# Optimization experiments

Hardware: AMD Instinct MI355X
Metric: run time of the kernel (lower is better)

Reference implementation:

```python
import jax, jax.numpy as jnp
import numpy as np

DIM = 128
N_CENTERS = 30
CUT_LO, CUT_HI = 0.0, 10.0
N_CONV = 3
NODE_VOCAB = 100
EDGE_VOCAB = 500
N_NODES = 50000
N_EDGES = 800000
N_GRAPHS = 100
DIM_E = DIM + N_CENTERS  # 158


def setup_inputs() -> dict:
    key = jax.random.key(0)
    ks = jax.random.split(key, 20)
    def xav(k, shape):
        fan_in = shape[-2] if len(shape) >= 2 else shape[-1]
        return (jax.random.normal(k, shape, dtype=jnp.float32) / np.sqrt(fan_in)).astype(jnp.float32)
    inp = {
        'node_types': jax.random.randint(ks[0], (N_NODES,), 0, NODE_VOCAB),
        'edge_types': jax.random.randint(ks[1], (N_EDGES,), 0, EDGE_VOCAB),
        'src': jax.random.randint(ks[2], (N_EDGES,), 0, N_NODES),
        'dst': jax.random.randint(ks[3], (N_EDGES,), 0, N_NODES),
        'graph_ids': jnp.sort(jax.random.randint(ks[4], (N_NODES,), 0, N_GRAPHS)),
        'distances': jax.random.uniform(ks[5], (N_EDGES,), dtype=jnp.float32, minval=CUT_LO, maxval=CUT_HI),
        'n_graphs': N_GRAPHS,
        # embedding tables
        'node_emb': xav(ks[6], (NODE_VOCAB, DIM)),
        'edge_emb': xav(ks[7], (EDGE_VOCAB, DIM)),
        # stacked per-conv-layer weights (n_conv leading dim)
        'Wn1': xav(ks[8], (N_CONV, DIM, DIM)),  'bn1': jnp.zeros((N_CONV, DIM), jnp.float32),
        'Wn2': xav(ks[9], (N_CONV, DIM, DIM)),  'bn2': jnp.zeros((N_CONV, DIM), jnp.float32),
        'We1': xav(ks[10], (N_CONV, DIM_E, DIM)), 'be1': jnp.zeros((N_CONV, DIM), jnp.float32),
        'We2': xav(ks[11], (N_CONV, DIM, DIM)),  'be2': jnp.zeros((N_CONV, DIM), jnp.float32),
        'Wc':  xav(ks[12], (N_CONV, DIM, DIM)),  'bc': jnp.zeros((N_CONV, DIM), jnp.float32),
        # read layer
        'Wr1': xav(ks[13], (DIM, DIM)), 'br1': jnp.zeros((DIM,), jnp.float32),
        'Wr2': xav(ks[14], (DIM, 1)),   'br2': jnp.zeros((1,), jnp.float32),
    }
    return inp


def reference(node_types, edge_types, src, dst, graph_ids, distances, n_graphs,
              node_emb, edge_emb, Wn1, bn1, Wn2, bn2, We1, be1, We2, be2, Wc, bc,
              Wr1, br1, Wr2, br2):
    # embeddings
    h = node_emb[node_types]                      # [N, D]
    e_emb = edge_emb[edge_types]                  # [E, D]
    # RBF expansion of distances
    centers = jnp.linspace(CUT_LO, CUT_HI, N_CENTERS, dtype=jnp.float32)
    gap = centers[1] - centers[0]
    rbf = jnp.exp(-((distances[:, None] - centers[None, :]) ** 2) / gap)  # [E, n_centers]
    e = jnp.concatenate([e_emb, rbf], axis=1)     # [E, D + n_centers]

    n_nodes = h.shape[0]
    for i in range(N_CONV):
        node_path = jnp.maximum(h[src] @ Wn1[i] + bn1[i], 0.0) @ Wn2[i] + bn2[i]   # [E, D]
        edge_path = jnp.maximum(e @ We1[i] + be1[i], 0.0) @ We2[i] + be2[i]        # [E, D]
        m = jnp.tanh((node_path * edge_path) @ Wc[i] + bc[i])                       # [E, D]
        h = h + jax.ops.segment_sum(m, dst, num_segments=n_nodes)                   # scatter-add to dst

    # readout MLP + per-graph node sum
    hr = jnp.maximum(h @ Wr1 + br1, 0.0) @ Wr2 + br2                                # [N, 1]
    out = jax.ops.segment_sum(hr, graph_ids, num_segments=n_graphs)                 # [G, 1]
    return out.reshape(-1)
```

## Files before the change

### kernel.cpp

```cpp
#include <hip/hip_runtime.h>
#include <stdint.h>

#define NNODES 50000
#define NEDGES 800000
#define NGRAPH 100
#define NCHUNK (NEDGES / 16)
#define NWAVES 4096

typedef _Float16 f16;
typedef __attribute__((ext_vector_type(8))) _Float16 half8;
typedef __attribute__((ext_vector_type(4))) _Float16 half4;
typedef __attribute__((ext_vector_type(4))) float floatx4;

__device__ __forceinline__ void stage_WT(const float* __restrict__ W, f16* WT,
                                         int tid, int nthr) {
    for (int idx = tid; idx < 128 * 32; idx += nthr) {
        int k = idx >> 5, n4 = (idx & 31) * 4;
        floatx4 v = *(const floatx4*)(W + k * 128 + n4);
        WT[(n4 + 0) * 136 + k] = (f16)v[0];
        WT[(n4 + 1) * 136 + k] = (f16)v[1];
        WT[(n4 + 2) * 136 + k] = (f16)v[2];
        WT[(n4 + 3) * 136 + k] = (f16)v[3];
    }
}

__device__ __forceinline__ float fast_tanh(float x) {
    x = fminf(fmaxf(x, -15.0f), 15.0f);
    float e2 = __expf(2.0f * x);
    return (e2 - 1.0f) * __builtin_amdgcn_rcpf(e2 + 1.0f);
}

__device__ __forceinline__ int mtAddr(int c, int rgroup) {
    return c * 16 + ((((c >> 2) + rgroup) & 3) << 2);
}

__global__ void init_k(float* out, int osz, int* cnt) {
    int i = blockIdx.x * 256 + threadIdx.x;
    if (i < osz) out[i] = 0.0f;
    if (i < NNODES) cnt[i] = 0;
}

__global__ void hist_k(const int* __restrict__ dst, int* __restrict__ cnt) {
    int e = blockIdx.x * 256 + threadIdx.x;
    if (e < NEDGES) atomicAdd(&cnt[dst[e]], 1);
}

__global__ __launch_bounds__(1024) void scan1_k(const int* __restrict__ cnt,
                                                int* __restrict__ rowStart,
                                                int* __restrict__ blockSum) {
    __shared__ int buf[1024];
    int tid = threadIdx.x;
    int i = blockIdx.x * 1024 + tid;
    int v = (i < NNODES) ? cnt[i] : 0;
    buf[tid] = v;
    __syncthreads();
    for (int off = 1; off < 1024; off <<= 1) {
        int t = (tid >= off) ? buf[tid - off] : 0;
        __syncthreads();
        buf[tid] += t;
        __syncthreads();
    }
    if (i < NNODES) rowStart[i] = buf[tid] - v;
    if (tid == 1023) blockSum[blockIdx.x] = buf[1023];
}

__global__ void scan2_k(int* __restrict__ blockSum, int nb) {
    if (threadIdx.x == 0) {
        int run = 0;
        for (int b = 0; b < nb; ++b) { int s = blockSum[b]; blockSum[b] = run; run += s; }
    }
}

__global__ __launch_bounds__(1024) void scan3_k(int* __restrict__ rowStart,
                                                const int* __restrict__ blockSum,
                                                int* __restrict__ cnt) {
    int i = blockIdx.x * 1024 + threadIdx.x;
    if (i < NNODES) { rowStart[i] += blockSum[blockIdx.x]; cnt[i] = 0; }
    if (i == 0) rowStart[NNODES] = NEDGES;
}

__global__ void scatter_k(const int* __restrict__ src, const int* __restrict__ et,
                          const int* __restrict__ dst, const float* __restrict__ dist,
                          const int* __restrict__ rowStart, int* __restrict__ cnt,
                          uint4* __restrict__ packE) {
    int e = blockIdx.x * 256 + threadIdx.x;
    if (e >= NEDGES) return;
    int d = dst[e];
    int pos = rowStart[d] + atomicAdd(&cnt[d], 1);
    uint4 pk;
    pk.x = (unsigned)src[e];
    pk.y = (unsigned)et[e];
    pk.z = (unsigned)d;
    pk.w = __float_as_uint(dist[e]);
    packE[pos] = pk;
}

__global__ void gather_h(const int* __restrict__ nt, const float* __restrict__ emb,
                         float* __restrict__ h) {
    int i = blockIdx.x * 256 + threadIdx.x;
    int row = i >> 5, c4 = (i & 31) * 4;
    if (row < NNODES)
        *(floatx4*)(h + row * 128 + c4) = *(const floatx4*)(emb + nt[row] * 128 + c4);
}

template <int MODE>
__global__ __launch_bounds__(1024, 4) void mlp_kernel(
        const float* __restrict__ X, int M,
        const float* __restrict__ W1, const float* __restrict__ b1,
        const float* __restrict__ W2, const float* __restrict__ b2,
        f16* __restrict__ Out) {
    __shared__ f16 W1T[128 * 136];
    __shared__ f16 W2T[(MODE == 0) ? 128 * 136 : 8];
    __shared__ f16 xBuf[256 * 136];
    __shared__ float bias1[128];
    __shared__ float bias2[128];
    int tid = threadIdx.x;

    stage_WT(W1, W1T, tid, 1024);
    if (MODE == 0) stage_WT(W2, W2T, tid, 1024);
    if (tid < 128) { bias1[tid] = b1[tid]; bias2[tid] = (MODE == 0) ? b2[tid] : 0.0f; }

    int r0 = blockIdx.x * 256;
    for (int it = 0; it < 8; ++it) {
        int row = it * 32 + (tid >> 5);
        int c4 = (tid & 31) * 4;
        int gr = r0 + row;
        floatx4 x = {0.0f, 0.0f, 0.0f, 0.0f};
        if (gr < M) x = *(const floatx4*)(X + (size_t)gr * 128 + c4);
        f16* dph = xBuf + row * 136 + c4;
        dph[0] = (f16)x[0]; dph[1] = (f16)x[1]; dph[2] = (f16)x[2]; dph[3] = (f16)x[3];
    }
    __syncthreads();

    int lane = tid & 63, wv = tid >> 6;
    int R = wv * 16;
    int n16 = lane & 15, q = lane >> 4;

    half8 a[4];
    #pragma unroll
    for (int kk = 0; kk < 4; ++kk)
        a[kk] = *(const half8*)(xBuf + (R + n16) * 136 + kk * 32 + q * 8);

    floatx4 acc[8];
    #pragma unroll
    for (int f = 0; f < 8; ++f) {
        float bb = bias1[f * 16 + n16];
        acc[f] = (floatx4){bb, bb, bb, bb};
        #pragma unroll
        for (int kk = 0; kk < 4; ++kk) {
            half8 b = *(const half8*)(W1T + (f * 16 + n16) * 136 + kk * 32 + q * 8);
            acc[f] = __builtin_amdgcn_mfma_f32_16x16x32_f16(a[kk], b, acc[f], 0, 0, 0);
        }
    }

    if (MODE == 0) {
        #pragma unroll
        for (int f = 0; f < 8; ++f)
            #pragma unroll
            for (int i = 0; i < 4; ++i)
                xBuf[(R + q * 4 + i) * 136 + f * 16 + n16] = (f16)fmaxf(acc[f][i], 0.0f);
        #pragma unroll
        for (int kk = 0; kk < 4; ++kk)
            a[kk] = *(const half8*)(xBuf + (R + n16) * 136 + kk * 32 + q * 8);
        #pragma unroll
        for (int f = 0; f < 8; ++f) {
            float bb = bias2[f * 16 + n16];
            acc[f] = (floatx4){bb, bb, bb, bb};
            #pragma unroll
            for (int kk = 0; kk < 4; ++kk) {
                half8 b = *(const half8*)(W2T + (f * 16 + n16) * 136 + kk * 32 + q * 8);
                acc[f] = __builtin_amdgcn_mfma_f32_16x16x32_f16(a[kk], b, acc[f], 0, 0, 0);
            }
        }
        #pragma unroll
        for (int f = 0; f < 8; ++f)
            #pragma unroll
            for (int i = 0; i < 4; ++i) {
                int gr = r0 + R + q * 4 + i;
                if (gr < M) Out[(size_t)gr * 128 + f * 16 + n16] = (f16)acc[f][i];
            }
    } else {
        #pragma unroll
        for (int f = 0; f < 8; ++f)
            #pragma unroll
            for (int i = 0; i < 4; ++i) {
                int gr = r0 + R + q * 4 + i;
                if (gr < M) Out[(size_t)gr * 128 + f * 16 + n16] = (f16)acc[f][i];
            }
    }
}

__global__ __launch_bounds__(1024, 4) void edge_kernel(
        const uint4* __restrict__ packE,
        const f16* __restrict__ P, const f16* __restrict__ T,
        const float* __restrict__ We1,
        const float* __restrict__ We2, const float* __restrict__ be2,
        const float* __restrict__ Wc,  const float* __restrict__ bc,
        float* __restrict__ h) {
    __shared__ f16 W2T[128 * 136];
    __shared__ f16 WcT[128 * 136];
    __shared__ f16 W1rT[128 * 40];
    __shared__ f16 Uall[16 * 2176];
    __shared__ float sbe2[128], sbc[128];
    __shared__ int dstW[16][16];

    int tid = threadIdx.x;
    stage_WT(We2, W2T, tid, 1024);
    stage_WT(Wc,  WcT, tid, 1024);
    for (int idx = tid; idx < 128 * 32; idx += 1024) {
        int n = idx >> 5, kr = idx & 31;
        W1rT[n * 40 + kr] = (kr < 30) ? (f16)We1[(128 + kr) * 128 + n] : (f16)0.0f;
    }
    if (tid < 128) { sbe2[tid] = be2[tid]; sbc[tid] = bc[tid]; }
    __syncthreads();

    int lane = tid & 63, wv = tid >> 6;
    f16* U = Uall + wv * 2176;
    int* dW = dstW[wv];
    int n16 = lane & 15, q = lane >> 4;
    const float invgap = 29.0f / 10.0f;
    int colA = lane, colB = lane + 64;

    int wgid = blockIdx.x * 16 + wv;
    const int CPW = (NCHUNK + NWAVES - 1) / NWAVES;
    int c0 = wgid * CPW;
    int c1 = c0 + CPW; if (c1 > NCHUNK) c1 = NCHUNK;

    float carry0 = 0.0f, carry1 = 0.0f;
    int prev = -1;

    for (int ch = c0; ch < c1; ++ch) {
        int e0 = ch * 16;
        uint4 pk = {0u, 0u, 0u, 0u};
        if (lane < 16) pk = packE[e0 + lane];
        int   ety  = __shfl((int)pk.y, lane >> 2);
        int   srcv = __shfl((int)pk.x, n16);
        float d    = __shfl(__uint_as_float(pk.w), n16);
        if (lane < 16) dW[lane] = (int)pk.z;
        {
            int row = lane >> 2, sub = lane & 3;
            const uint4* Tp = (const uint4*)(T + (size_t)ety * 128 + sub * 32);
            uint4* ub = (uint4*)(U + row * 136 + sub * 32);
            ub[0] = Tp[0]; ub[1] = Tp[1]; ub[2] = Tp[2]; ub[3] = Tp[3];
        }
        half8 pA[4];
        {
            const f16* Pr = P + (size_t)srcv * 128 + q * 8;
            #pragma unroll
            for (int kk = 0; kk < 4; ++kk) pA[kk] = *(const half8*)(Pr + kk * 32);
        }

        {
            half8 ar;
            #pragma unroll
            for (int j = 0; j < 8; ++j) {
                int k = q * 8 + j;
                float c = (float)k * (10.0f / 29.0f);
                float df = d - c;
                ar[j] = (f16)((k < 30) ? __expf(-df * df * invgap) : 0.0f);
            }
            #pragma unroll
            for (int f = 0; f < 8; ++f) {
                int col = f * 16 + n16;
                floatx4 c4;
                #pragma unroll
                for (int i = 0; i < 4; ++i) c4[i] = (float)U[(q * 4 + i) * 136 + col];
                half8 br = *(const half8*)(W1rT + col * 40 + q * 8);
                c4 = __builtin_amdgcn_mfma_f32_16x16x32_f16(ar, br, c4, 0, 0, 0);
                #pragma unroll
                for (int i = 0; i < 4; ++i)
                    U[(q * 4 + i) * 136 + col] = (f16)fmaxf(c4[i], 0.0f);
            }
        }

        half8 a2[4];
        #pragma unroll
        for (int kk = 0; kk < 4; ++kk)
            a2[kk] = *(const half8*)(U + n16 * 136 + kk * 32 + q * 8);
        floatx4 ep[8];
        #pragma unroll
        for (int f = 0; f < 8; ++f) {
            float bb = sbe2[f * 16 + n16];
            ep[f] = (floatx4){bb, bb, bb, bb};
            #pragma unroll
            for (int kk = 0; kk < 4; ++kk) {
                half8 b = *(const half8*)(W2T + (f * 16 + n16) * 136 + kk * 32 + q * 8);
                ep[f] = __builtin_amdgcn_mfma_f32_16x16x32_f16(a2[kk], b, ep[f], 0, 0, 0);
            }
        }

        #pragma unroll
        for (int f = 0; f < 8; ++f) {
            int col = f * 16 + n16;
            #pragma unroll
            for (int i = 0; i < 4; ++i)
                U[(q * 4 + i) * 136 + col] = (f16)ep[f][i];
        }

        #pragma unroll
        for (int kk = 0; kk < 4; ++kk) {
            half8 pe = *(const half8*)(U + n16 * 136 + kk * 32 + q * 8);
            a2[kk] = pe * pA[kk];
        }
        floatx4 mm[8];
        #pragma unroll
        for (int f = 0; f < 8; ++f) {
            float bb = sbc[f * 16 + n16];
            mm[f] = (floatx4){bb, bb, bb, bb};
            #pragma unroll
            for (int kk = 0; kk < 4; ++kk) {
                half8 b = *(const half8*)(WcT + (f * 16 + n16) * 136 + kk * 32 + q * 8);
                mm[f] = __builtin_amdgcn_mfma_f32_16x16x32_f16(a2[kk], b, mm[f], 0, 0, 0);
            }
        }
        #pragma unroll
        for (int f = 0; f < 8; ++f) {
            int c = f * 16 + n16;
            half4 mv;
            #pragma unroll
            for (int i = 0; i < 4; ++i) mv[i] = (f16)fast_tanh(mm[f][i]);
            *(half4*)(U + mtAddr(c, q)) = mv;
        }

        {
            half4 va[4], vb[4];
            #pragma unroll
            for (int g2 = 0; g2 < 4; ++g2) {
                va[g2] = *(const half4*)(U + mtAddr(colA, g2));
                vb[g2] = *(const half4*)(U + mtAddr(colB, g2));
            }
            int dArr[16];
            *(int4*)(dArr)      = *(const int4*)(dW);
            *(int4*)(dArr + 4)  = *(const int4*)(dW + 4);
            *(int4*)(dArr + 8)  = *(const int4*)(dW + 8);
            *(int4*)(dArr + 12) = *(const int4*)(dW + 12);
            #pragma unroll
            for (int r = 0; r < 16; ++r) {
                int dd = dArr[r];
                float v0 = (float)va[r >> 2][r & 3];
                float v1 = (float)vb[r >> 2][r & 3];
                if (dd != prev) {
                    if (prev >= 0) {
                        unsafeAtomicAdd(&h[(size_t)prev * 128 + colA], carry0);
                        unsafeAtomicAdd(&h[(size_t)prev * 128 + colB], carry1);
                    }
                    prev = dd; carry0 = v0; carry1 = v1;
                } else { carry0 += v0; carry1 += v1; }
            }
        }
    }
    if (prev >= 0) {
        unsafeAtomicAdd(&h[(size_t)prev * 128 + colA], carry0);
        unsafeAtomicAdd(&h[(size_t)prev * 128 + colB], carry1);
    }
}

__global__ __launch_bounds__(1024, 4) void readout_k(
        const float* __restrict__ X, int M,
        const float* __restrict__ W1, const float* __restrict__ b1,
        const float* __restrict__ Wr2, const float* __restrict__ br2,
        const int* __restrict__ gid, float* __restrict__ out) {
    __shared__ f16 W1T[128 * 136];
    __shared__ f16 xBuf[256 * 136];
    __shared__ float bias1[128];
    __shared__ float sWr2[128];
    int tid = threadIdx.x;

    stage_WT(W1, W1T, tid, 1024);
    if (tid < 128) { bias1[tid] = b1[tid]; sWr2[tid] = Wr2[tid]; }

    int r0 = blockIdx.x * 256;
    for (int it = 0; it < 8; ++it) {
        int row = it * 32 + (tid >> 5);
        int c4 = (tid & 31) * 4;
        int gr = r0 + row;
        floatx4 x = {0.0f, 0.0f, 0.0f, 0.0f};
        if (gr < M) x = *(const floatx4*)(X + (size_t)gr * 128 + c4);
        f16* dph = xBuf + row * 136 + c4;
        dph[0] = (f16)x[0]; dph[1] = (f16)x[1]; dph[2] = (f16)x[2]; dph[3] = (f16)x[3];
    }
    __syncthreads();

    int lane = tid & 63, wv = tid >> 6;
    int R = wv * 16;
    int n16 = lane & 15, q = lane >> 4;

    half8 a[4];
    #pragma unroll
    for (int kk = 0; kk < 4; ++kk)
        a[kk] = *(const half8*)(xBuf + (R + n16) * 136 + kk * 32 + q * 8);

    floatx4 acc[8];
    #pragma unroll
    for (int f = 0; f < 8; ++f) {
        float bb = bias1[f * 16 + n16];
        acc[f] = (floatx4){bb, bb, bb, bb};
        #pragma unroll
        for (int kk = 0; kk < 4; ++kk) {
            half8 b = *(const half8*)(W1T + (f * 16 + n16) * 136 + kk * 32 + q * 8);
            acc[f] = __builtin_amdgcn_mfma_f32_16x16x32_f16(a[kk], b, acc[f], 0, 0, 0);
        }
    }

    float s[4];
    #pragma unroll
    for (int i = 0; i < 4; ++i) {
        float t = 0.0f;
        #pragma unroll
        for (int f = 0; f < 8; ++f)
            t += fmaxf(acc[f][i], 0.0f) * sWr2[f * 16 + n16];
        #pragma unroll
        for (int m = 1; m < 16; m <<= 1) t += __shfl_xor(t, m);
        s[i] = t;
    }

    if (n16 == 0) {
        float br2v = br2[0];
        float t = 0.0f; int g = -1;
        #pragma unroll
        for (int i = 0; i < 4; ++i) {
            int gr = r0 + R + q * 4 + i;
            if (gr < M) {
                int gi = gid[gr];
                float si = s[i] + br2v;
                if (gi == g) t += si;
                else { if (g >= 0) unsafeAtomicAdd(&out[g], t); g = gi; t = si; }
            }
        }
        if (g >= 0) unsafeAtomicAdd(&out[g], t);
    }
}

extern "C" void kernel_launch(void* const* d_in, const int* in_sizes, int n_in,
                              void* d_out, int out_size, void* d_ws, size_t ws_size,
                              hipStream_t stream) {
    (void)in_sizes; (void)n_in; (void)ws_size;
    const int*   node_types = (const int*)d_in[0];
    const int*   edge_types = (const int*)d_in[1];
    const int*   src        = (const int*)d_in[2];
    const int*   dst        = (const int*)d_in[3];
    const int*   graph_ids  = (const int*)d_in[4];
    const float* distances  = (const float*)d_in[5];
    const float* node_emb   = (const float*)d_in[7];
    const float* edge_emb   = (const float*)d_in[8];
    const float* Wn1 = (const float*)d_in[9];
    const float* bn1 = (const float*)d_in[10];
    const float* Wn2 = (const float*)d_in[11];
    const float* bn2 = (const float*)d_in[12];
    const float* We1 = (const float*)d_in[13];
    const float* be1 = (const float*)d_in[14];
    const float* We2 = (const float*)d_in[15];
    const float* be2 = (const float*)d_in[16];
    const float* Wc  = (const float*)d_in[17];
    const float* bc  = (const float*)d_in[18];
    const float* Wr1 = (const float*)d_in[19];
    const float* br1 = (const float*)d_in[20];
    const float* Wr2 = (const float*)d_in[21];
    const float* br2 = (const float*)d_in[22];

    char* w = (char*)d_ws;
    auto carve = [&](size_t bytes) { char* p = w; w += (bytes + 255) & ~(size_t)255; return p; };
    float* h        = (float*)carve((size_t)NNODES * 128 * 4);
    f16*   P        = (f16*)  carve((size_t)NNODES * 128 * 2);
    f16*   T        = (f16*)  carve((size_t)500 * 128 * 2);
    int*   rowStart = (int*)  carve((size_t)(NNODES + 1) * 4);
    int*   cnt      = (int*)  carve((size_t)NNODES * 4);
    int*   blockSum = (int*)  carve((size_t)64 * 4);
    uint4* packE    = (uint4*)carve((size_t)NEDGES * 16);

    float* out = (float*)d_out;
    const int NB1 = (NNODES + 1023) / 1024;

    init_k<<<(NNODES + 255) / 256, 256, 0, stream>>>(out, out_size, cnt);
    hist_k<<<NEDGES / 256, 256, 0, stream>>>(dst, cnt);
    scan1_k<<<NB1, 1024, 0, stream>>>(cnt, rowStart, blockSum);
    scan2_k<<<1, 64, 0, stream>>>(blockSum, NB1);
    scan3_k<<<NB1, 1024, 0, stream>>>(rowStart, blockSum, cnt);
    scatter_k<<<NEDGES / 256, 256, 0, stream>>>(src, edge_types, dst, distances,
                                                rowStart, cnt, packE);
    gather_h<<<(NNODES * 32 + 255) / 256, 256, 0, stream>>>(node_types, node_emb, h);

    for (int i = 0; i < 3; ++i) {
        mlp_kernel<2><<<(500 + 255) / 256, 1024, 0, stream>>>(
            edge_emb, 500, We1 + (size_t)i * 158 * 128, be1 + i * 128, nullptr, nullptr, T);
        mlp_kernel<0><<<(NNODES + 255) / 256, 1024, 0, stream>>>(
            h, NNODES, Wn1 + (size_t)i * 128 * 128, bn1 + i * 128,
            Wn2 + (size_t)i * 128 * 128, bn2 + i * 128, P);
        edge_kernel<<<256, 1024, 0, stream>>>(
            packE, P, T,
            We1 + (size_t)i * 158 * 128,
            We2 + (size_t)i * 128 * 128, be2 + i * 128,
            Wc + (size_t)i * 128 * 128, bc + i * 128, h);
    }

    readout_k<<<(NNODES + 255) / 256, 1024, 0, stream>>>(
        h, NNODES, Wr1, br1, Wr2, br2, graph_ids, out);
}
```

Baseline: 735.6 us.

## Prefetch next edge chunk gathers and transpose MFMA operands for vectorized stores

The edge kernel now software-pipelines its per-chunk gathers. While the current chunk is computed, the next chunk's packed edge record, edge-type table row and source-node P row are loaded into registers, hiding global-memory latency. The MFMA operands are swapped so each lane holds four consecutive output columns, which turns the scalar LDS and global writes into half4 vector stores and lets the epilogue fuse into the GEMM loop without keeping eight accumulators live. Chunk distribution is also rebalanced to an exact 12-or-13 split. The trade-off is extra registers for the prefetched data, which may pressure occupancy under the 1024-thread launch bounds.

```diff
diff --git a/kernel.cpp b/kernel.cpp
--- a/kernel.cpp
+++ b/kernel.cpp
@@ -127,66 +127,60 @@
         int gr = r0 + row;
         floatx4 x = {0.0f, 0.0f, 0.0f, 0.0f};
         if (gr < M) x = *(const floatx4*)(X + (size_t)gr * 128 + c4);
-        f16* dph = xBuf + row * 136 + c4;
-        dph[0] = (f16)x[0]; dph[1] = (f16)x[1]; dph[2] = (f16)x[2]; dph[3] = (f16)x[3];
+        half4 xh;
+        xh[0] = (f16)x[0]; xh[1] = (f16)x[1]; xh[2] = (f16)x[2]; xh[3] = (f16)x[3];
+        *(half4*)(xBuf + row * 136 + c4) = xh;
     }
     __syncthreads();
 
     int lane = tid & 63, wv = tid >> 6;
     int R = wv * 16;
     int n16 = lane & 15, q = lane >> 4;
+    int gr = r0 + R + n16;
 
     half8 a[4];
     #pragma unroll
     for (int kk = 0; kk < 4; ++kk)
         a[kk] = *(const half8*)(xBuf + (R + n16) * 136 + kk * 32 + q * 8);
 
-    floatx4 acc[8];
     #pragma unroll
     for (int f = 0; f < 8; ++f) {
-        float bb = bias1[f * 16 + n16];
-        acc[f] = (floatx4){bb, bb, bb, bb};
+        floatx4 acc = *(const floatx4*)(bias1 + f * 16 + q * 4);
         #pragma unroll
         for (int kk = 0; kk < 4; ++kk) {
-            half8 b = *(const half8*)(W1T + (f * 16 + n16) * 136 + kk * 32 + q * 8);
-            acc[f] = __builtin_amdgcn_mfma_f32_16x16x32_f16(a[kk], b, acc[f], 0, 0, 0);
+            half8 aw = *(const half8*)(W1T + (f * 16 + n16) * 136 + kk * 32 + q * 8);
+            acc = __builtin_amdgcn_mfma_f32_16x16x32_f16(aw, a[kk], acc, 0, 0, 0);
+        }
+        if (MODE == 0) {
+            half4 y;
+            #pragma unroll
+            for (int i = 0; i < 4; ++i) y[i] = (f16)fmaxf(acc[i], 0.0f);
+            *(half4*)(xBuf + (R + n16) * 136 + f * 16 + q * 4) = y;
+        } else {
+            half4 o;
+            #pragma unroll
+            for (int i = 0; i < 4; ++i) o[i] = (f16)acc[i];
+            if (gr < M) *(half4*)(Out + (size_t)gr * 128 + f * 16 + q * 4) = o;
         }
     }
 
     if (MODE == 0) {
-        #pragma unroll
-        for (int f = 0; f < 8; ++f)
-            #pragma unroll
-            for (int i = 0; i < 4; ++i)
-                xBuf[(R + q * 4 + i) * 136 + f * 16 + n16] = (f16)fmaxf(acc[f][i], 0.0f);
         #pragma unroll
         for (int kk = 0; kk < 4; ++kk)
             a[kk] = *(const half8*)(xBuf + (R + n16) * 136 + kk * 32 + q * 8);
         #pragma unroll
         for (int f = 0; f < 8; ++f) {
-            float bb = bias2[f * 16 + n16];
-            acc[f] = (floatx4){bb, bb, bb, bb};
+            floatx4 acc = *(const floatx4*)(bias2 + f * 16 + q * 4);
             #pragma unroll
             for (int kk = 0; kk < 4; ++kk) {
-                half8 b = *(const half8*)(W2T + (f * 16 + n16) * 136 + kk * 32 + q * 8);
-                acc[f] = __builtin_amdgcn_mfma_f32_16x16x32_f16(a[kk], b, acc[f], 0, 0, 0);
+                half8 aw = *(const half8*)(W2T + (f * 16 + n16) * 136 + kk * 32 + q * 8);
+                acc = __builtin_amdgcn_mfma_f32_16x16x32_f16(aw, a[kk], acc, 0, 0, 0);
             }
-        }
-        #pragma unroll
-        for (int f = 0; f < 8; ++f)
-            #pragma unroll
-            for (int i = 0; i < 4; ++i) {
-                int gr = r0 + R + q * 4 + i;
-                if (gr < M) Out[(size_t)gr * 128 + f * 16 + n16] = (f16)acc[f][i];
-            }
-    } else {
-        #pragma unroll
-        for (int f = 0; f < 8; ++f)
-            #pragma unroll
-            for (int i = 0; i < 4; ++i) {
-                int gr = r0 + R + q * 4 + i;
-                if (gr < M) Out[(size_t)gr * 128 + f * 16 + n16] = (f16)acc[f][i];
-            }
+            half4 o;
+            #pragma unroll
+            for (int i = 0; i < 4; ++i) o[i] = (f16)acc[i];
+            if (gr < M) *(half4*)(Out + (size_t)gr * 128 + f * 16 + q * 4) = o;
+        }
     }
 }
 
@@ -220,105 +214,126 @@
     int n16 = lane & 15, q = lane >> 4;
     const float invgap = 29.0f / 10.0f;
     int colA = lane, colB = lane + 64;
+    int tsub = lane & 3, trow = lane >> 2;
+
+    float sbcv[8];
+    #pragma unroll
+    for (int f = 0; f < 8; ++f) sbcv[f] = sbc[f * 16 + n16];
 
     int wgid = blockIdx.x * 16 + wv;
-    const int CPW = (NCHUNK + NWAVES - 1) / NWAVES;
-    int c0 = wgid * CPW;
-    int c1 = c0 + CPW; if (c1 > NCHUNK) c1 = NCHUNK;
+    int extra = wgid < 848 ? wgid : 848;
+    int c0 = wgid * 12 + extra;
+    int c1 = c0 + 12 + (wgid < 848 ? 1 : 0);
 
     float carry0 = 0.0f, carry1 = 0.0f;
     int prev = -1;
 
+    uint4 pk = {0u, 0u, 0u, 0u};
+    if (lane < 16) pk = packE[(size_t)c0 * 16 + lane];
+    int   ety  = __shfl((int)pk.y, trow);
+    int   srcv = __shfl((int)pk.x, n16);
+    float dcur = __shfl(__uint_as_float(pk.w), n16);
+    int   dstv = (int)pk.z;
+    uint4 tr0, tr1, tr2, tr3;
+    {
+        const uint4* Tp = (const uint4*)(T + (size_t)ety * 128 + tsub * 32);
+        tr0 = Tp[0]; tr1 = Tp[1]; tr2 = Tp[2]; tr3 = Tp[3];
+    }
+    half8 pA0, pA1, pA2, pA3;
+    {
+        const f16* Pr = P + (size_t)srcv * 128 + q * 8;
+        pA0 = *(const half8*)(Pr);
+        pA1 = *(const half8*)(Pr + 32);
+        pA2 = *(const half8*)(Pr + 64);
+        pA3 = *(const half8*)(Pr + 96);
+    }
+
     for (int ch = c0; ch < c1; ++ch) {
-        int e0 = ch * 16;
-        uint4 pk = {0u, 0u, 0u, 0u};
-        if (lane < 16) pk = packE[e0 + lane];
-        int   ety  = __shfl((int)pk.y, lane >> 2);
-        int   srcv = __shfl((int)pk.x, n16);
-        float d    = __shfl(__uint_as_float(pk.w), n16);
-        if (lane < 16) dW[lane] = (int)pk.z;
+        bool hasNext = (ch + 1 < c1);
+        if (lane < 16) dW[lane] = dstv;
         {
-            int row = lane >> 2, sub = lane & 3;
-            const uint4* Tp = (const uint4*)(T + (size_t)ety * 128 + sub * 32);
-            uint4* ub = (uint4*)(U + row * 136 + sub * 32);
-            ub[0] = Tp[0]; ub[1] = Tp[1]; ub[2] = Tp[2]; ub[3] = Tp[3];
-        }
-        half8 pA[4];
-        {
-            const f16* Pr = P + (size_t)srcv * 128 + q * 8;
-            #pragma unroll
-            for (int kk = 0; kk < 4; ++kk) pA[kk] = *(const half8*)(Pr + kk * 32);
-        }
-
-        {
-            half8 ar;
-            #pragma unroll
-            for (int j = 0; j < 8; ++j) {
-                int k = q * 8 + j;
-                float c = (float)k * (10.0f / 29.0f);
-                float df = d - c;
-                ar[j] = (f16)((k < 30) ? __expf(-df * df * invgap) : 0.0f);
-            }
-            #pragma unroll
-            for (int f = 0; f < 8; ++f) {
-                int col = f * 16 + n16;
-                floatx4 c4;
-                #pragma unroll
-                for (int i = 0; i < 4; ++i) c4[i] = (float)U[(q * 4 + i) * 136 + col];
-                half8 br = *(const half8*)(W1rT + col * 40 + q * 8);
-                c4 = __builtin_amdgcn_mfma_f32_16x16x32_f16(ar, br, c4, 0, 0, 0);
-                #pragma unroll
-                for (int i = 0; i < 4; ++i)
-                    U[(q * 4 + i) * 136 + col] = (f16)fmaxf(c4[i], 0.0f);
-            }
+            uint4* ub = (uint4*)(U + trow * 136 + tsub * 32);
+            ub[0] = tr0; ub[1] = tr1; ub[2] = tr2; ub[3] = tr3;
+        }
+        uint4 pkn = {0u, 0u, 0u, 0u};
+        if (hasNext && lane < 16) pkn = packE[(size_t)(ch + 1) * 16 + lane];
+
+        half8 ar;
+        #pragma unroll
+        for (int j = 0; j < 8; ++j) {
+            int k = q * 8 + j;
+            float c = (float)k * (10.0f / 29.0f);
+            float df = dcur - c;
+            ar[j] = (f16)((k < 30) ? __expf(-df * df * invgap) : 0.0f);
+        }
+        #pragma unroll
+        for (int f = 0; f < 8; ++f) {
+            f16* up = U + n16 * 136 + f * 16 + q * 4;
+            half4 tv = *(const half4*)up;
+            floatx4 c4 = {(float)tv[0], (float)tv[1], (float)tv[2], (float)tv[3]};
+            half8 aw = *(const half8*)(W1rT + (f * 16 + n16) * 40 + q * 8);
+            c4 = __builtin_amdgcn_mfma_f32_16x16x32_f16(aw, ar, c4, 0, 0, 0);
+            half4 uv;
+            #pragma unroll
+            for (int i = 0; i < 4; ++i) uv[i] = (f16)fmaxf(c4[i], 0.0f);
+            *(half4*)up = uv;
         }
 
         half8 a2[4];
         #pragma unroll
         for (int kk = 0; kk < 4; ++kk)
             a2[kk] = *(const half8*)(U + n16 * 136 + kk * 32 + q * 8);
-        floatx4 ep[8];
         #pragma unroll
         for (int f = 0; f < 8; ++f) {
-            float bb = sbe2[f * 16 + n16];
-            ep[f] = (floatx4){bb, bb, bb, bb};
+            floatx4 acc = *(const floatx4*)(sbe2 + f * 16 + q * 4);
             #pragma unroll
             for (int kk = 0; kk < 4; ++kk) {
-                half8 b = *(const half8*)(W2T + (f * 16 + n16) * 136 + kk * 32 + q * 8);
-                ep[f] = __builtin_amdgcn_mfma_f32_16x16x32_f16(a2[kk], b, ep[f], 0, 0, 0);
+                half8 aw = *(const half8*)(W2T + (f * 16 + n16) * 136 + kk * 32 + q * 8);
+                acc = __builtin_amdgcn_mfma_f32_16x16x32_f16(aw, a2[kk], acc, 0, 0, 0);
             }
-        }
-
+            half4 ev;
+            #pragma unroll
+            for (int i = 0; i < 4; ++i) ev[i] = (f16)acc[i];
+            *(half4*)(U + n16 * 136 + f * 16 + q * 4) = ev;
+        }
+
+        int   etyn = __shfl((int)pkn.y, trow);
+        int   srcn = __shfl((int)pkn.x, n16);
+        float dn   = __shfl(__uint_as_float(pkn.w), n16);
+        uint4 trn0, trn1, trn2, trn3;
+        {
+            const uint4* Tp = (const uint4*)(T + (size_t)etyn * 128 + tsub * 32);
+            trn0 = Tp[0]; trn1 = Tp[1]; trn2 = Tp[2]; trn3 = Tp[3];
+        }
+        half8 pB0, pB1, pB2, pB3;
+        {
+            const f16* Pr = P + (size_t)srcn * 128 + q * 8;
+            pB0 = *(const half8*)(Pr);
+            pB1 = *(const half8*)(Pr + 32);
+            pB2 = *(const half8*)(Pr + 64);
+            pB3 = *(const half8*)(Pr + 96);
+        }
+
+        {
+            half8 e0 = *(const half8*)(U + n16 * 136 + 0 * 32 + q * 8);
+            half8 e1 = *(const half8*)(U + n16 * 136 + 1 * 32 + q * 8);
+            half8 e2 = *(const half8*)(U + n16 * 136 + 2 * 32 + q * 8);
+            half8 e3 = *(const half8*)(U + n16 * 136 + 3 * 32 + q * 8);
+            a2[0] = e0 * pA0; a2[1] = e1 * pA1; a2[2] = e2 * pA2; a2[3] = e3 * pA3;
+        }
         #pragma unroll
         for (int f = 0; f < 8; ++f) {
-            int col = f * 16 + n16;
-            #pragma unroll
-            for (int i = 0; i < 4; ++i)
-                U[(q * 4 + i) * 136 + col] = (f16)ep[f][i];
-        }
-
-        #pragma unroll
-        for (int kk = 0; kk < 4; ++kk) {
-            half8 pe = *(const half8*)(U + n16 * 136 + kk * 32 + q * 8);
-            a2[kk] = pe * pA[kk];
-        }
-        floatx4 mm[8];
-        #pragma unroll
-        for (int f = 0; f < 8; ++f) {
-            float bb = sbc[f * 16 + n16];
-            mm[f] = (floatx4){bb, bb, bb, bb};
+            float bb = sbcv[f];
+            floatx4 acc = {bb, bb, bb, bb};
             #pragma unroll
             for (int kk = 0; kk < 4; ++kk) {
                 half8 b = *(const half8*)(WcT + (f * 16 + n16) * 136 + kk * 32 + q * 8);
-                mm[f] = __builtin_amdgcn_mfma_f32_16x16x32_f16(a2[kk], b, mm[f], 0, 0, 0);
+                acc = __builtin_amdgcn_mfma_f32_16x16x32_f16(a2[kk], b, acc, 0, 0, 0);
             }
-        }
-        #pragma unroll
-        for (int f = 0; f < 8; ++f) {
             int c = f * 16 + n16;
             half4 mv;
             #pragma unroll
-            for (int i = 0; i < 4; ++i) mv[i] = (f16)fast_tanh(mm[f][i]);
+            for (int i = 0; i < 4; ++i) mv[i] = (f16)fast_tanh(acc[i]);
             *(half4*)(U + mtAddr(c, q)) = mv;
         }
 
@@ -348,6 +363,10 @@
                 } else { carry0 += v0; carry1 += v1; }
             }
         }
+
+        tr0 = trn0; tr1 = trn1; tr2 = trn2; tr3 = trn3;
+        pA0 = pB0; pA1 = pB1; pA2 = pB2; pA3 = pB3;
+        dcur = dn; dstv = (int)pkn.z;
     }
     if (prev >= 0) {
         unsafeAtomicAdd(&h[(size_t)prev * 128 + colA], carry0);
@@ -376,8 +395,9 @@
         int gr = r0 + row;
         floatx4 x = {0.0f, 0.0f, 0.0f, 0.0f};
         if (gr < M) x = *(const floatx4*)(X + (size_t)gr * 128 + c4);
-        f16* dph = xBuf + row * 136 + c4;
-        dph[0] = (f16)x[0]; dph[1] = (f16)x[1]; dph[2] = (f16)x[2]; dph[3] = (f16)x[3];
+        half4 xh;
+        xh[0] = (f16)x[0]; xh[1] = (f16)x[1]; xh[2] = (f16)x[2]; xh[3] = (f16)x[3];
+        *(half4*)(xBuf + row * 136 + c4) = xh;
     }
     __syncthreads();
 
```

Result: slower. 839.8 us (+14.2%).
